# Performance work log

Measured on AMD Instinct MI355X. Metric: run time of the kernel, lower is better.

Reference implementation:

```python
import jax, jax.numpy as jnp
import numpy as np

NUM_TYPES = 60
TOK_DIM = 128
DIM_TOK = TOK_DIM + 1          # +1 sentinel bucket
SMALL = 2
C = NUM_TYPES + DIM_TOK + SMALL  # 191 channels
STEPS = 10
BLOCKS = 5
NTYPES_E = 3
N = 4000
E = 12000
G = 32
LN_EPS = 1e-5


def setup_inputs() -> dict:
    key = jax.random.key(0)
    ks = jax.random.split(key, 12)
    p = lambda k, shape: jax.random.normal(k, shape, dtype=jnp.float32) * 0.02
    return dict(
        x_small=jax.random.uniform(ks[0], (N, SMALL), dtype=jnp.float32),
        conv_w=p(ks[1], (BLOCKS, NTYPES_E, STEPS, C, C)),
        gru_wih=p(ks[2], (BLOCKS, NTYPES_E, 3 * C, C)),
        gru_whh=p(ks[3], (BLOCKS, NTYPES_E, 3 * C, C)),
        gru_bih=jnp.zeros((BLOCKS, NTYPES_E, 3 * C), jnp.float32),
        gru_bhh=jnp.zeros((BLOCKS, NTYPES_E, 3 * C), jnp.float32),
        ln_w=jnp.ones((BLOCKS, C), jnp.float32),
        ln_b=jnp.zeros((BLOCKS, C), jnp.float32),
        head_w1=p(ks[4], (C, C)),
        head_b1=jnp.zeros((C,), jnp.float32),
        head_w2=p(ks[5], (C, 2)),
        head_b2=jnp.zeros((2,), jnp.float32),
        x_type=jax.random.randint(ks[6], (N,), 0, NUM_TYPES),
        x_tok=jax.random.randint(ks[7], (N,), 0, DIM_TOK),
        edge_index=jax.random.randint(ks[8], (2, E), 0, N),
        edge_type=jax.random.randint(ks[9], (E,), 0, NTYPES_E),
        batch=jnp.sort(jax.random.randint(ks[10], (N,), 0, G)),
    )


def reference(x_small, conv_w, gru_wih, gru_whh, gru_bih, gru_bhh,
              ln_w, ln_b, head_w1, head_b1, head_w2, head_b2,
              x_type, x_tok, edge_index, edge_type, batch):
    n = x_type.shape[0]
    # build_features: one-hot type || one-hot hashed token || small floats
    h_type = jax.nn.one_hot(x_type, NUM_TYPES, dtype=jnp.float32)
    h_tok = jax.nn.one_hot(jnp.clip(x_tok, 0, DIM_TOK - 1), DIM_TOK, dtype=jnp.float32)
    h = jnp.concatenate([h_type, h_tok, x_small], axis=1)  # [N, C]
    src, dst = edge_index[0], edge_index[1]

    def gated_conv(h0, w_steps, wih, whh, bih, bhh, emask):
        # PyG GatedGraphConv: per step, m = x @ W_i; scatter-add m[src]->dst; x = GRUCell(agg, x)
        def step(x, wi):
            m = x @ wi  # [N, C]
            agg = jax.ops.segment_sum(m[src] * emask[:, None], dst, num_segments=n)
            gi = agg @ wih.T + bih  # [N, 3C] input gates (r,z,n order as in torch)
            gh = x @ whh.T + bhh
            ir, iz, ic = jnp.split(gi, 3, axis=-1)
            hr, hz, hc = jnp.split(gh, 3, axis=-1)
            r = jax.nn.sigmoid(ir + hr)
            z = jax.nn.sigmoid(iz + hz)
            c = jnp.tanh(ic + r * hc)
            return (1.0 - z) * c + z * x, None
        x, _ = jax.lax.scan(step, h0, w_steps)
        return x

    for b in range(BLOCKS):
        h_msg = jnp.zeros_like(h)
        for t in range(NTYPES_E):
            # edge-type masking as zero-weight scatter (same math as boolean slicing)
            emask = (edge_type == t).astype(h.dtype)
            h_msg = h_msg + gated_conv(h, conv_w[b, t], gru_wih[b, t], gru_whh[b, t],
                                       gru_bih[b, t], gru_bhh[b, t], emask)
        x = h + h_msg
        mu = jnp.mean(x, axis=-1, keepdims=True)
        var = jnp.mean((x - mu) ** 2, axis=-1, keepdims=True)
        h = jax.nn.relu((x - mu) * jax.lax.rsqrt(var + LN_EPS) * ln_w[b] + ln_b[b])
        # dropout is identity in eval mode

    # global_mean_pool
    counts = jax.ops.segment_sum(jnp.ones((n,), h.dtype), batch, num_segments=G)
    hg = jax.ops.segment_sum(h, batch, num_segments=G) / jnp.maximum(counts, 1.0)[:, None]
    z1 = jax.nn.relu(hg @ head_w1 + head_b1)
    return z1 @ head_w2 + head_b2  # [G, 2] logits
```

## Files before the change

### kernel.cpp

```cpp
#include <hip/hip_runtime.h>
#include <math.h>

#define N_NODES 4000
#define CC 191
#define CP 192
#define NT 3
#define NB 5
#define NS 10
#define EE 12000
#define GG 32
#define THREE_C 573
#define NC (N_NODES * CP)
#define NPAD 576

typedef __attribute__((ext_vector_type(8))) short short8;
typedef __attribute__((ext_vector_type(4))) float f32x4;

__device__ __forceinline__ unsigned short f2bf(float f) {
    unsigned u = __float_as_uint(f);
    unsigned r = (u + 0x7fffu + ((u >> 16) & 1u)) >> 16;
    return (unsigned short)r;
}
__device__ __forceinline__ float bf2f(unsigned short s) {
    return __uint_as_float(((unsigned)s) << 16);
}
__device__ __forceinline__ float dot4(float4 a, float4 b) {
    return a.x * b.x + a.y * b.y + a.z * b.z + a.w * b.w;
}

__global__ void k_build_h(const float* __restrict__ xs, const int* __restrict__ xtype,
                          const int* __restrict__ xtok, float* __restrict__ h) {
    int idx = blockIdx.x * 256 + threadIdx.x;
    if (idx >= NC) return;
    int i = idx / CP, c = idx % CP;
    float v = 0.f;
    if (c < 60) {
        v = (xtype[i] == c) ? 1.f : 0.f;
    } else if (c < 189) {
        int tk = xtok[i];
        tk = tk < 0 ? 0 : (tk > 128 ? 128 : tk);
        v = (tk == c - 60) ? 1.f : 0.f;
    } else if (c < CC) {
        v = xs[i * 2 + (c - 189)];
    }
    h[idx] = v;
}

__global__ void k_pad_conv(const float* __restrict__ w, float* __restrict__ wp) {
    long idx = (long)blockIdx.x * 256 + threadIdx.x;
    if (idx >= 150L * 192 * 192) return;
    int b = (int)(idx / (192 * 192));
    int r = (int)((idx / 192) % 192);
    int c = (int)(idx % 192);
    wp[idx] = (r < CC && c < CC) ? w[(long)b * CC * CC + (long)r * CC + c] : 0.f;
}

__global__ void k_pad573(const float* __restrict__ w, float* __restrict__ wp, int batches) {
    long tot = (long)batches * THREE_C * CP;
    long idx = (long)blockIdx.x * 256 + threadIdx.x;
    if (idx >= tot) return;
    int b = (int)(idx / (THREE_C * CP));
    int r = (int)((idx / CP) % THREE_C);
    int c = (int)(idx % CP);
    wp[idx] = (c < CC) ? w[((long)b * THREE_C + r) * CC + c] : 0.f;
}

__global__ void k_edge_count(const int* __restrict__ ei, const int* __restrict__ et,
                             int* __restrict__ cnt) {
    int e = blockIdx.x * 256 + threadIdx.x;
    if (e >= EE) return;
    atomicAdd(&cnt[et[e] * N_NODES + ei[EE + e]], 1);
}

__global__ void k_scan(const int* __restrict__ cnt, int* __restrict__ off, int* __restrict__ fill) {
    const int TOT = NT * N_NODES;
    const int CH = (TOT + 255) / 256;
    __shared__ int ls[256];
    int tid = threadIdx.x;
    int base = tid * CH;
    int s = 0;
    for (int u = 0; u < CH; u++) {
        int idx = base + u;
        if (idx < TOT) s += cnt[idx];
    }
    ls[tid] = s;
    __syncthreads();
    for (int d = 1; d < 256; d <<= 1) {
        int v = 0;
        if (tid >= d) v = ls[tid - d];
        __syncthreads();
        if (tid >= d) ls[tid] += v;
        __syncthreads();
    }
    int run = (tid > 0) ? ls[tid - 1] : 0;
    for (int u = 0; u < CH; u++) {
        int idx = base + u;
        if (idx < TOT) {
            off[idx] = run;
            fill[idx] = run;
            run += cnt[idx];
        }
    }
    if (tid == 255) off[TOT] = run;
}

__global__ void k_edge_fill(const int* __restrict__ ei, const int* __restrict__ et,
                            int* __restrict__ fill, int* __restrict__ csrc) {
    int e = blockIdx.x * 256 + threadIdx.x;
    if (e >= EE) return;
    int pos = atomicAdd(&fill[et[e] * N_NODES + ei[EE + e]], 1);
    csrc[pos] = ei[e];
}

__global__ __launch_bounds__(256) void k_fmat(const float* __restrict__ wih_p,
                                              const float* __restrict__ conv_wp,
                                              float* __restrict__ F_t, int b) {
    int ts = blockIdx.z;
    int t = ts / NS;
    int j30 = blockIdx.x * 32;
    int k0 = blockIdx.y * 64;
    const float* A = wih_p + (long)(b * 3 + t) * THREE_C * CP;
    const float* B = conv_wp + ((long)b * 30 + ts) * 192 * 192;
    __shared__ float sA[32 * 52];
    __shared__ float sB[64 * 52];
    int tid = threadIdx.x;
    int tj = tid % 32;
    int tn = tid / 32;
    float acc0[4] = {0, 0, 0, 0}, acc1[4] = {0, 0, 0, 0};
    for (int kb = 0; kb < 4; kb++) {
        int q0 = kb * 48;
        for (int idx = tid; idx < 32 * 12; idx += 256) {
            int row = idx / 12, c4 = idx % 12;
            int j3 = j30 + row; j3 = j3 < THREE_C ? j3 : THREE_C - 1;
            *(float4*)(sA + row * 52 + c4 * 4) = *(const float4*)(A + (long)j3 * CP + q0 + c4 * 4);
        }
        for (int idx = tid; idx < 64 * 12; idx += 256) {
            int row = idx / 12, c4 = idx % 12;
            *(float4*)(sB + row * 52 + c4 * 4) = *(const float4*)(B + (long)(k0 + row) * CP + q0 + c4 * 4);
        }
        __syncthreads();
        #pragma unroll 3
        for (int q4 = 0; q4 < 12; q4++) {
            float4 bv0 = *(const float4*)(sB + tj * 52 + q4 * 4);
            float4 bv1 = *(const float4*)(sB + (tj + 32) * 52 + q4 * 4);
            #pragma unroll
            for (int u = 0; u < 4; u++) {
                float4 av = *(const float4*)(sA + (tn + 8 * u) * 52 + q4 * 4);
                acc0[u] += dot4(av, bv0);
                acc1[u] += dot4(av, bv1);
            }
        }
        __syncthreads();
    }
    #pragma unroll
    for (int u = 0; u < 4; u++) {
        int j3 = j30 + tn + 8 * u;
        if (j3 < THREE_C) {
            F_t[((long)ts * THREE_C + j3) * CP + k0 + tj] = acc0[u];
            F_t[((long)ts * THREE_C + j3) * CP + k0 + tj + 32] = acc1[u];
        }
    }
}

__global__ void k_convF(const float* __restrict__ F_t, unsigned short* __restrict__ FH,
                        unsigned short* __restrict__ FL) {
    long idx = (long)blockIdx.x * 256 + threadIdx.x;
    if (idx >= 30L * NPAD * CP) return;
    int k = (int)(idx % CP);
    int p = (int)((idx / CP) % NPAD);
    int ts = (int)(idx / ((long)NPAD * CP));
    float v = 0.f;
    if (p < THREE_C) {
        int j = p / 3, g = p % 3;
        v = F_t[((long)ts * THREE_C + g * CC + j) * CP + k];
    }
    unsigned short hi = f2bf(v);
    FH[idx] = hi;
    FL[idx] = f2bf(v - bf2f(hi));
}

__global__ void k_convW(const float* __restrict__ whh_p, unsigned short* __restrict__ WH,
                        unsigned short* __restrict__ WL, int b) {
    long idx = (long)blockIdx.x * 256 + threadIdx.x;
    if (idx >= 3L * NPAD * CP) return;
    int k = (int)(idx % CP);
    int p = (int)((idx / CP) % NPAD);
    int t = (int)(idx / ((long)NPAD * CP));
    float v = 0.f;
    if (p < THREE_C) {
        int j = p / 3, g = p % 3;
        v = whh_p[((long)(b * 3 + t) * THREE_C + g * CC + j) * CP + k];
    }
    unsigned short hi = f2bf(v);
    WH[idx] = hi;
    WL[idx] = f2bf(v - bf2f(hi));
}

__global__ void k_split3(const float* __restrict__ h, unsigned short* __restrict__ XH,
                         unsigned short* __restrict__ XL) {
    int idx = blockIdx.x * 256 + threadIdx.x;
    if (idx >= NC) return;
    float f = h[idx];
    unsigned short hi = f2bf(f);
    unsigned short lo = f2bf(f - bf2f(hi));
    #pragma unroll
    for (int t = 0; t < NT; t++) {
        XH[(long)t * NC + idx] = hi;
        XL[(long)t * NC + idx] = lo;
    }
}

__global__ void k_agg(const unsigned short* __restrict__ XH, const unsigned short* __restrict__ XL,
                      unsigned short* __restrict__ AH, unsigned short* __restrict__ AL,
                      const int* __restrict__ off, const int* __restrict__ csrc) {
    int node = blockIdx.x;
    int t = blockIdx.y;
    int k = threadIdx.x;
    const unsigned short* Xh = XH + (long)t * NC;
    const unsigned short* Xl = XL + (long)t * NC;
    int e0 = off[t * N_NODES + node];
    int e1 = off[t * N_NODES + node + 1];
    float s = 0.f;
    for (int e = e0; e < e1; e++) {
        long base = (long)csrc[e] * CP + k;
        s += bf2f(Xh[base]) + bf2f(Xl[base]);
    }
    unsigned short hi = f2bf(s);
    long o = ((long)t * N_NODES + node) * CP + k;
    AH[o] = hi;
    AL[o] = f2bf(s - bf2f(hi));
}

__global__ __launch_bounds__(256, 2) void k_step(
        const unsigned short* __restrict__ XcH, const unsigned short* __restrict__ XcL,
        const unsigned short* __restrict__ AH, const unsigned short* __restrict__ AL,
        const unsigned short* __restrict__ FH, const unsigned short* __restrict__ FL,
        const unsigned short* __restrict__ WH, const unsigned short* __restrict__ WL,
        const float* __restrict__ bih, const float* __restrict__ bhh,
        unsigned short* __restrict__ XnH, unsigned short* __restrict__ XnL,
        int b, int s) {
    const int t = blockIdx.z;
    const int ts = t * NS + s;
    const int M0 = blockIdx.x * 128;
    const int N0 = blockIdx.y * 96;

    __shared__ __align__(16) char smem[35840];
    unsigned short* sX = (unsigned short*)smem;
    unsigned short* sG = sX + 5120;
    unsigned short* sF = sG + 5120;
    unsigned short* sW = sF + 3840;

    const int tid = threadIdx.x;
    const int lane = tid & 63;
    const int wave = tid >> 6;
    const int wm = wave & 1;
    const int wn = wave >> 1;
    const int l15 = lane & 15;
    const int kb = lane >> 4;

    f32x4 accGI[4][3], accGH[4][3];
    #pragma unroll
    for (int mi = 0; mi < 4; mi++)
        #pragma unroll
        for (int nj = 0; nj < 3; nj++) {
            accGI[mi][nj] = (f32x4){0.f, 0.f, 0.f, 0.f};
            accGH[mi][nj] = (f32x4){0.f, 0.f, 0.f, 0.f};
        }

    for (int ks = 0; ks < 18; ks++) {
        int ako, bko;
        const unsigned short *Xs, *Gs, *Fs, *Ws;
        if (ks < 6)       { ako = ks * 32;        Xs = XcH; Gs = AH; bko = ks * 32;        Fs = FH; Ws = WH; }
        else if (ks < 12) { ako = (ks - 6) * 32;  Xs = XcL; Gs = AL; bko = (ks - 6) * 32;  Fs = FH; Ws = WH; }
        else              { ako = (ks - 12) * 32; Xs = XcH; Gs = AH; bko = (ks - 12) * 32; Fs = FL; Ws = WL; }

        __syncthreads();
        #pragma unroll
        for (int it = 0; it < 2; it++) {
            int idx = tid + it * 256;
            int row = idx >> 2, q = idx & 3;
            int node = M0 + row; node = node < N_NODES ? node : N_NODES - 1;
            size_t go = (size_t)(t * N_NODES + node) * CP + ako + q * 8;
            *(uint4*)(sX + row * 40 + q * 8) = *(const uint4*)(Xs + go);
            *(uint4*)(sG + row * 40 + q * 8) = *(const uint4*)(Gs + go);
        }
        {
            int idx = tid;
            if (idx < 384) {
                int row = idx >> 2, q = idx & 3;
                size_t fo = (size_t)(ts * NPAD + N0 + row) * CP + bko + q * 8;
                size_t wo = (size_t)(t * NPAD + N0 + row) * CP + bko + q * 8;
                *(uint4*)(sF + row * 40 + q * 8) = *(const uint4*)(Fs + fo);
                *(uint4*)(sW + row * 40 + q * 8) = *(const uint4*)(Ws + wo);
            }
            idx = tid + 256;
            if (idx < 384) {
                int row = idx >> 2, q = idx & 3;
                size_t fo = (size_t)(ts * NPAD + N0 + row) * CP + bko + q * 8;
                size_t wo = (size_t)(t * NPAD + N0 + row) * CP + bko + q * 8;
                *(uint4*)(sF + row * 40 + q * 8) = *(const uint4*)(Fs + fo);
                *(uint4*)(sW + row * 40 + q * 8) = *(const uint4*)(Ws + wo);
            }
        }
        __syncthreads();

        short8 xa[4], ga[4], fb[3], wb[3];
        #pragma unroll
        for (int mi = 0; mi < 4; mi++) {
            int r = wm * 64 + mi * 16 + l15;
            xa[mi] = *(const short8*)(sX + r * 40 + kb * 8);
            ga[mi] = *(const short8*)(sG + r * 40 + kb * 8);
        }
        #pragma unroll
        for (int nj = 0; nj < 3; nj++) {
            int r = wn * 48 + nj * 16 + l15;
            fb[nj] = *(const short8*)(sF + r * 40 + kb * 8);
            wb[nj] = *(const short8*)(sW + r * 40 + kb * 8);
        }
        #pragma unroll
        for (int mi = 0; mi < 4; mi++)
            #pragma unroll
            for (int nj = 0; nj < 3; nj++) {
                accGI[mi][nj] = __builtin_amdgcn_mfma_f32_16x16x32_bf16(
                    ga[mi], fb[nj], accGI[mi][nj], 0, 0, 0);
                accGH[mi][nj] = __builtin_amdgcn_mfma_f32_16x16x32_bf16(
                    xa[mi], wb[nj], accGH[mi][nj], 0, 0, 0);
            }
    }

    float* eGI = (float*)smem;
    float* eGH = eGI + 3200;
    const int c = tid & 15;
    const int rg = tid >> 4;
    const int bo = (b * 3 + t) * THREE_C;

    for (int p = 0; p < 4; p++) {
        __syncthreads();
        if (wave == p) {
            #pragma unroll
            for (int mi = 0; mi < 4; mi++)
                #pragma unroll
                for (int nj = 0; nj < 3; nj++)
                    #pragma unroll
                    for (int r = 0; r < 4; r++) {
                        int grow = mi * 16 + kb * 4 + r;
                        int gcol = nj * 16 + l15;
                        eGI[grow * 50 + gcol] = accGI[mi][nj][r];
                        eGH[grow * 50 + gcol] = accGH[mi][nj][r];
                    }
        }
        __syncthreads();
        int pm = p & 1, pn = p >> 1;
        int j = blockIdx.y * 32 + pn * 16 + c;
        float bir = 0, biz = 0, bic = 0, bhr = 0, bhz = 0, bhc = 0;
        if (j < CC) {
            bir = bih[bo + j]; biz = bih[bo + CC + j]; bic = bih[bo + 2 * CC + j];
            bhr = bhh[bo + j]; bhz = bhh[bo + CC + j]; bhc = bhh[bo + 2 * CC + j];
        }
        #pragma unroll
        for (int q = 0; q < 4; q++) {
            int lr = rg * 4 + q;
            int node = M0 + pm * 64 + lr;
            if (node >= N_NODES) continue;
            unsigned short oh = 0, ol = 0;
            if (j < CC) {
                float gir = eGI[lr * 50 + 3 * c], giz = eGI[lr * 50 + 3 * c + 1],
                      gic = eGI[lr * 50 + 3 * c + 2];
                float ghr = eGH[lr * 50 + 3 * c], ghz = eGH[lr * 50 + 3 * c + 1],
                      ghc = eGH[lr * 50 + 3 * c + 2];
                size_t xi = (size_t)(t * N_NODES + node) * CP + j;
                float xold = bf2f(XcH[xi]) + bf2f(XcL[xi]);
                float rr = 1.f / (1.f + expf(-(gir + bir + ghr + bhr)));
                float zz = 1.f / (1.f + expf(-(giz + biz + ghz + bhz)));
                float cg = tanhf(gic + bic + rr * (ghc + bhc));
                float outv = (1.f - zz) * cg + zz * xold;
                oh = f2bf(outv);
                ol = f2bf(outv - bf2f(oh));
            }
            size_t oi = (size_t)(t * N_NODES + node) * CP + j;
            XnH[oi] = oh;
            XnL[oi] = ol;
        }
    }
}

__global__ void k_ln(float* __restrict__ h, const unsigned short* __restrict__ XH,
                     const unsigned short* __restrict__ XL,
                     const float* __restrict__ lnw, const float* __restrict__ lnb, int b) {
    int i = blockIdx.x;
    int c = threadIdx.x;
    long base = (long)i * CP + c;
    float v = 0.f;
    if (c < CC) {
        v = h[base];
        #pragma unroll
        for (int t = 0; t < NT; t++)
            v += bf2f(XH[(long)t * NC + base]) + bf2f(XL[(long)t * NC + base]);
    }
    float sv = v;
    for (int o = 32; o > 0; o >>= 1) sv += __shfl_down(sv, o);
    __shared__ float ls[3];
    __shared__ float bc[2];
    if ((threadIdx.x & 63) == 0) ls[threadIdx.x >> 6] = sv;
    __syncthreads();
    if (threadIdx.x == 0) bc[0] = (ls[0] + ls[1] + ls[2]) / (float)CC;
    __syncthreads();
    float mu = bc[0];
    float d = (c < CC) ? (v - mu) : 0.f;
    float s2 = d * d;
    for (int o = 32; o > 0; o >>= 1) s2 += __shfl_down(s2, o);
    __syncthreads();
    if ((threadIdx.x & 63) == 0) ls[threadIdx.x >> 6] = s2;
    __syncthreads();
    if (threadIdx.x == 0) bc[1] = (ls[0] + ls[1] + ls[2]) / (float)CC;
    __syncthreads();
    float var = bc[1];
    float y = 0.f;
    if (c < CC) {
        y = d * rsqrtf(var + 1e-5f) * lnw[b * CC + c] + lnb[b * CC + c];
        y = y > 0.f ? y : 0.f;
    }
    h[base] = y;
}

__global__ void k_pool(const float* __restrict__ h, const int* __restrict__ batch,
                       float* __restrict__ hg, float* __restrict__ gcnt) {
    int idx = blockIdx.x * 256 + threadIdx.x;
    if (idx >= NC) return;
    int i = idx / CP, c = idx % CP;
    int g = batch[i];
    if (c < CC) atomicAdd(&hg[g * CP + c], h[idx]);
    if (c == 0) atomicAdd(&gcnt[g], 1.f);
}

__global__ void k_head1(const float* __restrict__ hg, const float* __restrict__ gcnt,
                        const float* __restrict__ w1, const float* __restrict__ b1,
                        float* __restrict__ z1) {
    int g = blockIdx.x;
    int jcol = threadIdx.x;
    if (jcol >= CC) return;
    float inv = 1.f / fmaxf(gcnt[g], 1.f);
    float acc = 0.f;
    for (int k = 0; k < CC; k++) acc += hg[g * CP + k] * inv * w1[k * CC + jcol];
    acc += b1[jcol];
    z1[g * CP + jcol] = fmaxf(acc, 0.f);
}

__global__ void k_head2(const float* __restrict__ z1, const float* __restrict__ w2,
                        const float* __restrict__ b2, float* __restrict__ out) {
    int idx = threadIdx.x;
    if (idx >= GG * 2) return;
    int g = idx / 2, o = idx % 2;
    float acc = 0.f;
    for (int k = 0; k < CC; k++) acc += z1[g * CP + k] * w2[k * 2 + o];
    out[g * 2 + o] = acc + b2[o];
}

extern "C" void kernel_launch(void* const* d_in, const int* in_sizes, int n_in,
                              void* d_out, int out_size, void* d_ws, size_t ws_size,
                              hipStream_t stream) {
    const float* xs   = (const float*)d_in[0];
    const float* conv = (const float*)d_in[1];
    const float* wih  = (const float*)d_in[2];
    const float* whh  = (const float*)d_in[3];
    const float* bih  = (const float*)d_in[4];
    const float* bhh  = (const float*)d_in[5];
    const float* lnw  = (const float*)d_in[6];
    const float* lnb  = (const float*)d_in[7];
    const float* hw1  = (const float*)d_in[8];
    const float* hb1  = (const float*)d_in[9];
    const float* hw2  = (const float*)d_in[10];
    const float* hb2  = (const float*)d_in[11];
    const int* xtype  = (const int*)d_in[12];
    const int* xtok   = (const int*)d_in[13];
    const int* ei     = (const int*)d_in[14];
    const int* et     = (const int*)d_in[15];
    const int* batch  = (const int*)d_in[16];
    float* out = (float*)d_out;

    char* ws = (char*)d_ws;
    size_t o = 0;
    auto alloc = [&](size_t nbytes) {
        size_t r = o;
        o = (o + nbytes + 255) & ~(size_t)255;
        return r;
    };
    float* h      = (float*)(ws + alloc((size_t)NC * 4));
    float* F_t    = (float*)(ws + alloc((size_t)30 * THREE_C * CP * 4));
    float* wih_p  = (float*)(ws + alloc((size_t)15 * THREE_C * CP * 4));
    float* whh_p  = (float*)(ws + alloc((size_t)15 * THREE_C * CP * 4));
    float* convp  = (float*)(ws + alloc((size_t)150 * 192 * 192 * 4));
    unsigned short* FH  = (unsigned short*)(ws + alloc((size_t)30 * NPAD * CP * 2));
    unsigned short* FL  = (unsigned short*)(ws + alloc((size_t)30 * NPAD * CP * 2));
    unsigned short* WH  = (unsigned short*)(ws + alloc((size_t)3 * NPAD * CP * 2));
    unsigned short* WL  = (unsigned short*)(ws + alloc((size_t)3 * NPAD * CP * 2));
    unsigned short* XAh = (unsigned short*)(ws + alloc((size_t)NT * NC * 2));
    unsigned short* XAl = (unsigned short*)(ws + alloc((size_t)NT * NC * 2));
    unsigned short* XBh = (unsigned short*)(ws + alloc((size_t)NT * NC * 2));
    unsigned short* XBl = (unsigned short*)(ws + alloc((size_t)NT * NC * 2));
    unsigned short* AggH = (unsigned short*)(ws + alloc((size_t)NT * NC * 2));
    unsigned short* AggL = (unsigned short*)(ws + alloc((size_t)NT * NC * 2));
    float* hg     = (float*)(ws + alloc((size_t)GG * CP * 4));
    float* gcnt   = (float*)(ws + alloc((size_t)GG * 4));
    float* z1buf  = (float*)(ws + alloc((size_t)GG * CP * 4));
    int* cnt      = (int*)(ws + alloc((size_t)NT * N_NODES * 4));
    int* offb     = (int*)(ws + alloc((size_t)(NT * N_NODES + 1) * 4));
    int* fillb    = (int*)(ws + alloc((size_t)NT * N_NODES * 4));
    int* csrc     = (int*)(ws + alloc((size_t)EE * 4));
    (void)ws_size; (void)n_in; (void)in_sizes; (void)out_size;

    hipMemsetAsync(cnt, 0, (size_t)NT * N_NODES * 4, stream);
    hipMemsetAsync(hg, 0, (size_t)GG * CP * 4, stream);
    hipMemsetAsync(gcnt, 0, (size_t)GG * 4, stream);

    k_build_h<<<(NC + 255) / 256, 256, 0, stream>>>(xs, xtype, xtok, h);
    k_pad_conv<<<(int)((150L * 192 * 192 + 255) / 256), 256, 0, stream>>>(conv, convp);
    k_pad573<<<(int)(((long)15 * THREE_C * CP + 255) / 256), 256, 0, stream>>>(wih, wih_p, 15);
    k_pad573<<<(int)(((long)15 * THREE_C * CP + 255) / 256), 256, 0, stream>>>(whh, whh_p, 15);
    k_edge_count<<<(EE + 255) / 256, 256, 0, stream>>>(ei, et, cnt);
    k_scan<<<1, 256, 0, stream>>>(cnt, offb, fillb);
    k_edge_fill<<<(EE + 255) / 256, 256, 0, stream>>>(ei, et, fillb, csrc);

    for (int b = 0; b < NB; b++) {
        dim3 fg((THREE_C + 31) / 32, 3, 30);
        k_fmat<<<fg, 256, 0, stream>>>(wih_p, convp, F_t, b);
        k_convF<<<(int)((30L * NPAD * CP + 255) / 256), 256, 0, stream>>>(F_t, FH, FL);
        k_convW<<<(int)((3L * NPAD * CP + 255) / 256), 256, 0, stream>>>(whh_p, WH, WL, b);
        k_split3<<<(NC + 255) / 256, 256, 0, stream>>>(h, XAh, XAl);
        unsigned short *curH = XAh, *curL = XAl, *nxtH = XBh, *nxtL = XBl;
        for (int s = 0; s < NS; s++) {
            k_agg<<<dim3(N_NODES, NT), CP, 0, stream>>>(curH, curL, AggH, AggL, offb, csrc);
            dim3 sg(32, 6, NT);
            k_step<<<sg, 256, 0, stream>>>(curH, curL, AggH, AggL, FH, FL, WH, WL,
                                           bih, bhh, nxtH, nxtL, b, s);
            unsigned short* t1 = curH; curH = nxtH; nxtH = t1;
            unsigned short* t2 = curL; curL = nxtL; nxtL = t2;
        }
        k_ln<<<N_NODES, CP, 0, stream>>>(h, XAh, XAl, lnw, lnb, b);
    }

    k_pool<<<(NC + 255) / 256, 256, 0, stream>>>(h, batch, hg, gcnt);
    k_head1<<<GG, CP, 0, stream>>>(hg, gcnt, hw1, hb1, z1buf);
    k_head2<<<1, 64, 0, stream>>>(z1buf, hw2, hb2, out);
}
```

Before: 3.111 ms.

## Stage hi/lo split operands together per K-chunk with XOR-swizzled LDS layout

Restructures the k_step GEMM loop so each of 6 K-chunks loads the hi and lo parts of both A operands and both B operands into shared memory at once, then issues all three split-bf16 MFMA products per tile. This replaces 18 separate chunk iterations and cuts the number of barrier pairs and redundant reloads of the hi operands from three to one. The unpadded LDS rows use an XOR swizzle on the 16-byte column index to avoid bank conflicts. In exchange it holds more fragment registers per iteration, which can pressure occupancy under the 256x2 launch bound.

```diff
diff --git a/kernel.cpp b/kernel.cpp
--- a/kernel.cpp
+++ b/kernel.cpp
@@ -233,7 +233,7 @@
 
 __global__ __launch_bounds__(256, 2) void k_step(
         const unsigned short* __restrict__ XcH, const unsigned short* __restrict__ XcL,
-        const unsigned short* __restrict__ AH, const unsigned short* __restrict__ AL,
+        const unsigned short* __restrict__ AgH, const unsigned short* __restrict__ AgL,
         const unsigned short* __restrict__ FH, const unsigned short* __restrict__ FL,
         const unsigned short* __restrict__ WH, const unsigned short* __restrict__ WL,
         const float* __restrict__ bih, const float* __restrict__ bhh,
@@ -244,11 +244,7 @@
     const int M0 = blockIdx.x * 128;
     const int N0 = blockIdx.y * 96;
 
-    __shared__ __align__(16) char smem[35840];
-    unsigned short* sX = (unsigned short*)smem;
-    unsigned short* sG = sX + 5120;
-    unsigned short* sF = sG + 5120;
-    unsigned short* sW = sF + 3840;
+    __shared__ __align__(16) unsigned short smem[28672];
 
     const int tid = threadIdx.x;
     const int lane = tid & 63;
@@ -258,6 +254,17 @@
     const int l15 = lane & 15;
     const int kb = lane >> 4;
 
+    const unsigned short* gA[4];
+    gA[0] = XcH + (size_t)t * NC;
+    gA[1] = AgH + (size_t)t * NC;
+    gA[2] = XcL + (size_t)t * NC;
+    gA[3] = AgL + (size_t)t * NC;
+    const unsigned short* gB[4];
+    gB[0] = FH + (size_t)ts * NPAD * CP;
+    gB[1] = WH + (size_t)t * NPAD * CP;
+    gB[2] = FL + (size_t)ts * NPAD * CP;
+    gB[3] = WL + (size_t)t * NPAD * CP;
+
     f32x4 accGI[4][3], accGH[4][3];
     #pragma unroll
     for (int mi = 0; mi < 4; mi++)
@@ -267,64 +274,69 @@
             accGH[mi][nj] = (f32x4){0.f, 0.f, 0.f, 0.f};
         }
 
-    for (int ks = 0; ks < 18; ks++) {
-        int ako, bko;
-        const unsigned short *Xs, *Gs, *Fs, *Ws;
-        if (ks < 6)       { ako = ks * 32;        Xs = XcH; Gs = AH; bko = ks * 32;        Fs = FH; Ws = WH; }
-        else if (ks < 12) { ako = (ks - 6) * 32;  Xs = XcL; Gs = AL; bko = (ks - 6) * 32;  Fs = FH; Ws = WH; }
-        else              { ako = (ks - 12) * 32; Xs = XcH; Gs = AH; bko = (ks - 12) * 32; Fs = FL; Ws = WL; }
-
-        __syncthreads();
-        #pragma unroll
-        for (int it = 0; it < 2; it++) {
-            int idx = tid + it * 256;
-            int row = idx >> 2, q = idx & 3;
-            int node = M0 + row; node = node < N_NODES ? node : N_NODES - 1;
-            size_t go = (size_t)(t * N_NODES + node) * CP + ako + q * 8;
-            *(uint4*)(sX + row * 40 + q * 8) = *(const uint4*)(Xs + go);
-            *(uint4*)(sG + row * 40 + q * 8) = *(const uint4*)(Gs + go);
-        }
-        {
-            int idx = tid;
-            if (idx < 384) {
-                int row = idx >> 2, q = idx & 3;
-                size_t fo = (size_t)(ts * NPAD + N0 + row) * CP + bko + q * 8;
-                size_t wo = (size_t)(t * NPAD + N0 + row) * CP + bko + q * 8;
-                *(uint4*)(sF + row * 40 + q * 8) = *(const uint4*)(Fs + fo);
-                *(uint4*)(sW + row * 40 + q * 8) = *(const uint4*)(Ws + wo);
-            }
-            idx = tid + 256;
-            if (idx < 384) {
-                int row = idx >> 2, q = idx & 3;
-                size_t fo = (size_t)(ts * NPAD + N0 + row) * CP + bko + q * 8;
-                size_t wo = (size_t)(t * NPAD + N0 + row) * CP + bko + q * 8;
-                *(uint4*)(sF + row * 40 + q * 8) = *(const uint4*)(Fs + fo);
-                *(uint4*)(sW + row * 40 + q * 8) = *(const uint4*)(Ws + wo);
-            }
-        }
-        __syncthreads();
-
-        short8 xa[4], ga[4], fb[3], wb[3];
+    for (int k = 0; k < 6; k++) {
+        const int ko = k * 32;
+        __syncthreads();
+        #pragma unroll
+        for (int i = 0; i < 8; i++) {
+            int c = tid + i * 256;
+            int a = c >> 9;
+            int r = (c >> 2) & 127;
+            int qs = c & 3;
+            int q = qs ^ ((r >> 1) & 3);
+            int node = M0 + r; node = node < N_NODES ? node : N_NODES - 1;
+            const unsigned short* gp = gA[a] + (size_t)node * CP + ko + q * 8;
+            *(uint4*)(smem + a * 4096 + (r * 4 + qs) * 8) = *(const uint4*)gp;
+        }
+        #pragma unroll
+        for (int i = 0; i < 6; i++) {
+            int c = tid + i * 256;
+            int a = c / 384;
+            int rem = c - a * 384;
+            int r = rem >> 2;
+            int qs = rem & 3;
+            int q = qs ^ ((r >> 1) & 3);
+            const unsigned short* gp = gB[a] + (size_t)(N0 + r) * CP + ko + q * 8;
+            *(uint4*)(smem + 16384 + a * 3072 + (r * 4 + qs) * 8) = *(const uint4*)gp;
+        }
+        __syncthreads();
+
+        short8 xh[4], gh[4], xl[4], gl[4];
         #pragma unroll
         for (int mi = 0; mi < 4; mi++) {
             int r = wm * 64 + mi * 16 + l15;
-            xa[mi] = *(const short8*)(sX + r * 40 + kb * 8);
-            ga[mi] = *(const short8*)(sG + r * 40 + kb * 8);
-        }
+            int sl = (r * 4 + (kb ^ ((r >> 1) & 3))) * 8;
+            xh[mi] = *(const short8*)(smem + sl);
+            gh[mi] = *(const short8*)(smem + 4096 + sl);
+            xl[mi] = *(const short8*)(smem + 8192 + sl);
+            gl[mi] = *(const short8*)(smem + 12288 + sl);
+        }
+        short8 fh[3], wh[3], fl[3], wl[3];
         #pragma unroll
         for (int nj = 0; nj < 3; nj++) {
             int r = wn * 48 + nj * 16 + l15;
-            fb[nj] = *(const short8*)(sF + r * 40 + kb * 8);
-            wb[nj] = *(const short8*)(sW + r * 40 + kb * 8);
+            int sl = (r * 4 + (kb ^ ((r >> 1) & 3))) * 8;
+            fh[nj] = *(const short8*)(smem + 16384 + sl);
+            wh[nj] = *(const short8*)(smem + 19456 + sl);
+            fl[nj] = *(const short8*)(smem + 22528 + sl);
+            wl[nj] = *(const short8*)(smem + 25600 + sl);
         }
         #pragma unroll
         for (int mi = 0; mi < 4; mi++)
             #pragma unroll
             for (int nj = 0; nj < 3; nj++) {
                 accGI[mi][nj] = __builtin_amdgcn_mfma_f32_16x16x32_bf16(
-                    ga[mi], fb[nj], accGI[mi][nj], 0, 0, 0);
+                    gh[mi], fh[nj], accGI[mi][nj], 0, 0, 0);
+                accGI[mi][nj] = __builtin_amdgcn_mfma_f32_16x16x32_bf16(
+                    gl[mi], fh[nj], accGI[mi][nj], 0, 0, 0);
+                accGI[mi][nj] = __builtin_amdgcn_mfma_f32_16x16x32_bf16(
+                    gh[mi], fl[nj], accGI[mi][nj], 0, 0, 0);
                 accGH[mi][nj] = __builtin_amdgcn_mfma_f32_16x16x32_bf16(
-                    xa[mi], wb[nj], accGH[mi][nj], 0, 0, 0);
+                    xh[mi], wh[nj], accGH[mi][nj], 0, 0, 0);
+                accGH[mi][nj] = __builtin_amdgcn_mfma_f32_16x16x32_bf16(
+                    xl[mi], wh[nj], accGH[mi][nj], 0, 0, 0);
+                accGH[mi][nj] = __builtin_amdgcn_mfma_f32_16x16x32_bf16(
+                    xh[mi], wl[nj], accGH[mi][nj], 0, 0, 0);
             }
     }
 
```

After: 3.946 ms. +26.8%, slower.
